# Kernel tuning notes

Measured on AMD Instinct MI355X. Metric: run time of the kernel, lower is better.

## Reference

```python
import jax, jax.numpy as jnp
import numpy as np

H = 256        # hidden_size
MAX_LEN = 200  # position table has MAX_LEN+1 rows
B = 4096       # number of sessions


def setup_inputs() -> dict:
    rng = np.random.RandomState(0)
    # ragged session lengths in [10, 100)
    seq_len = rng.randint(10, 100, size=B).astype(np.int64)
    T = int(seq_len.sum())
    # reverse positions: len-1, ..., 1, 0 per session (as the torch code uses)
    reverse_pos = np.concatenate([np.arange(l - 1, -1, -1) for l in seq_len]).astype(np.int64)

    key = jax.random.key(0)
    ks = jax.random.split(key, 8)
    def lin(k, fin, fout):
        # torch Linear init ~ U(-1/sqrt(fin), 1/sqrt(fin)); store as [fin, fout]
        lim = 1.0 / np.sqrt(fin)
        kw, kb = jax.random.split(k)
        W = jax.random.uniform(kw, (fin, fout), jnp.float32, -lim, lim)
        b = jax.random.uniform(kb, (fout,), jnp.float32, -lim, lim)
        return W, b

    hidden = jax.random.normal(ks[0], (T, H), jnp.float32)
    pos_table = jax.random.normal(ks[1], (MAX_LEN + 1, H), jnp.float32)
    W_pos, b_pos = lin(ks[2], 2 * H, H)   # W_pos_inter
    W1, b1 = lin(ks[3], H, H)             # W_1_inter
    W2, b2 = lin(ks[4], H, H)             # W_2_inter
    qw, qb = lin(ks[5], H, 1)             # q_inter

    return {
        "hidden": hidden,
        "pos_table": pos_table,
        "W_pos": W_pos, "b_pos": b_pos,
        "W1": W1, "b1": b1,
        "W2": W2, "b2": b2,
        "qw": qw, "qb": qb,
        "seq_len": jnp.asarray(seq_len),
        "reverse_pos": jnp.asarray(reverse_pos),
    }


def reference(hidden, pos_table, W_pos, b_pos, W1, b1, W2, b2, qw, qb, seq_len, reverse_pos):
    T = hidden.shape[0]
    nb = seq_len.shape[0]
    # segment id per token (sessions are contiguous)
    seg = jnp.repeat(jnp.arange(nb), seq_len, total_repeat_length=T)  # [T]
    # per-session mean, gathered back per token (v_mean_repeat_concat)
    sess_mean = jax.ops.segment_sum(hidden, seg, num_segments=nb)
    sess_mean = sess_mean / seq_len[:, None].astype(hidden.dtype)
    v_mean = sess_mean[seg]                                           # [T, H]
    # position-augmented hidden: tanh(W_pos_inter([hidden; pos_emb]))
    pos_emb = pos_table[reverse_pos]                                  # [T, H]
    pos_hidden = jnp.tanh(jnp.concatenate([hidden, pos_emb], -1) @ W_pos + b_pos)
    # alpha = q_inter(sigmoid(W_1_inter(v_mean) + W_2_inter(pos_hidden)))
    gate = jax.nn.sigmoid(v_mean @ W1 + b1 + pos_hidden @ W2 + b2)
    alpha = gate @ qw + qb                                            # [T, 1]
    # per-session weighted sum of hidden
    h_s = jax.ops.segment_sum(alpha * hidden, seg, num_segments=nb)   # [B, H]
    return h_s
```

## Files before the change

kernel.cpp:

```cpp
#include <hip/hip_runtime.h>
#include <hip/hip_bf16.h>
#include <stdint.h>

#define HD 256
#define BM 64
#define APAD 8
#define ASTRIDE (HD + APAD)

typedef __bf16 bf16x8 __attribute__((ext_vector_type(8)));
typedef float f32x4 __attribute__((ext_vector_type(4)));
typedef unsigned short ushort8v __attribute__((ext_vector_type(8)));
typedef unsigned short us4 __attribute__((ext_vector_type(4)));

__device__ __forceinline__ unsigned short f2bf(float f) {
    unsigned int x = __float_as_uint(f);
    unsigned int r = (x + 0x7FFFu + ((x >> 16) & 1u)) >> 16;
    return (unsigned short)r;
}

__global__ void prep_kernel(const int* __restrict__ seq_len, int* __restrict__ offsets, int B,
                            const float* __restrict__ Wp, const float* __restrict__ W1,
                            const float* __restrict__ W2,
                            unsigned short* __restrict__ WphT, unsigned short* __restrict__ WpbT,
                            unsigned short* __restrict__ W1T, unsigned short* __restrict__ W2T) {
    int tid = threadIdx.x;
    if (blockIdx.x == 0) {
        __shared__ int sums[256];
        int per = (B + 255) / 256;
        int b0 = tid * per;
        int local[32];
        int tot = 0;
        for (int i = 0; i < per && i < 32; ++i) {
            int b = b0 + i;
            int v = (b < B) ? seq_len[b] : 0;
            local[i] = tot;
            tot += v;
        }
        sums[tid] = tot;
        __syncthreads();
        for (int off = 1; off < 256; off <<= 1) {
            int v = (tid >= off) ? sums[tid - off] : 0;
            __syncthreads();
            sums[tid] += v;
            __syncthreads();
        }
        int start = sums[tid] - tot;
        for (int i = 0; i < per && i < 32; ++i) {
            int b = b0 + i;
            if (b < B) offsets[b] = start + local[i];
        }
        if (tid == 255) offsets[B] = sums[255];
    } else {
        __shared__ unsigned short tile[64][72];
        int bid = blockIdx.x - 1;
        const float* src;
        unsigned short* dst;
        int k0, n0, kk;
        if (bid < 32) {
            int tk = bid >> 2, tn = bid & 3;
            src = Wp; k0 = tk * 64; n0 = tn * 64;
            if (k0 < 256) { dst = WphT; kk = k0; }
            else          { dst = WpbT; kk = k0 - 256; }
        } else if (bid < 48) {
            int b2 = bid - 32;
            src = W1; k0 = (b2 >> 2) * 64; n0 = (b2 & 3) * 64;
            dst = W1T; kk = k0;
        } else {
            int b2 = bid - 48;
            src = W2; k0 = (b2 >> 2) * 64; n0 = (b2 & 3) * 64;
            dst = W2T; kk = k0;
        }
        {
            int col = tid & 63;
            int rbase = tid >> 6;
            #pragma unroll
            for (int i = 0; i < 16; ++i) {
                int lrow = rbase + 4 * i;
                tile[lrow][col] = f2bf(src[(size_t)(k0 + lrow) * HD + n0 + col]);
            }
        }
        __syncthreads();
        {
            int nl = tid >> 2;
            int kc0 = (tid & 3) * 16;
            #pragma unroll
            for (int j = 0; j < 4; ++j) {
                int kc = kc0 + 4 * j;
                us4 v;
                v[0] = tile[kc + 0][nl];
                v[1] = tile[kc + 1][nl];
                v[2] = tile[kc + 2][nl];
                v[3] = tile[kc + 3][nl];
                *reinterpret_cast<us4*>(dst + (size_t)(n0 + nl) * HD + kk + kc) = v;
            }
        }
    }
}

__global__ __launch_bounds__(256) void mean_kernel(
    const float* __restrict__ hidden, const int* __restrict__ offsets,
    unsigned short* __restrict__ mean_bf, unsigned short* __restrict__ hb,
    int* __restrict__ seg, int B) {
    int wave = threadIdx.x >> 6, lane = threadIdx.x & 63;
    int b = blockIdx.x * 4 + wave;
    if (b >= B) return;
    int s = offsets[b], e = offsets[b + 1];
    for (int t = s + lane; t < e; t += 64) seg[t] = b;
    int c4 = lane * 4;
    float4 acc = {0.f, 0.f, 0.f, 0.f};
    if (hb) {
        for (int t = s; t < e; ++t) {
            const float4 v = *reinterpret_cast<const float4*>(hidden + (size_t)t * HD + c4);
            acc.x += v.x; acc.y += v.y; acc.z += v.z; acc.w += v.w;
            us4 pk;
            pk[0] = f2bf(v.x); pk[1] = f2bf(v.y); pk[2] = f2bf(v.z); pk[3] = f2bf(v.w);
            *reinterpret_cast<us4*>(hb + (size_t)t * HD + c4) = pk;
        }
    } else {
        for (int t = s; t < e; ++t) {
            const float4 v = *reinterpret_cast<const float4*>(hidden + (size_t)t * HD + c4);
            acc.x += v.x; acc.y += v.y; acc.z += v.z; acc.w += v.w;
        }
    }
    float inv = 1.0f / (float)(e - s);
    us4 pk;
    pk[0] = f2bf(acc.x * inv);
    pk[1] = f2bf(acc.y * inv);
    pk[2] = f2bf(acc.z * inv);
    pk[3] = f2bf(acc.w * inv);
    *reinterpret_cast<us4*>(mean_bf + (size_t)b * HD + c4) = pk;
}

__global__ __launch_bounds__(256) void small_gemm_kernel(
    const unsigned short* __restrict__ mean_bf, int Mu, int nbu,
    const float* __restrict__ pos_table, int Mp,
    const unsigned short* __restrict__ W1T, const unsigned short* __restrict__ WpbT,
    const float* __restrict__ b1, const float* __restrict__ b2, const float* __restrict__ bp,
    float* __restrict__ u, float* __restrict__ P2) {
    __shared__ __align__(16) unsigned short As[16][ASTRIDE];
    int tid = threadIdx.x;
    bool isU = (int)blockIdx.x < nbu;
    int m0 = isU ? blockIdx.x * 16 : (blockIdx.x - nbu) * 16;
    int M  = isU ? Mu : Mp;
    const unsigned short* BT = isU ? W1T : WpbT;
    float* out = isU ? u : P2;

    {
        int row = tid >> 4;
        int colg = (tid & 15) * 16;
        int m = m0 + row;
        if (isU) {
            ushort8v v0 = {0,0,0,0,0,0,0,0}, v1 = {0,0,0,0,0,0,0,0};
            if (m < M) {
                v0 = *reinterpret_cast<const ushort8v*>(mean_bf + (size_t)m * HD + colg);
                v1 = *reinterpret_cast<const ushort8v*>(mean_bf + (size_t)m * HD + colg + 8);
            }
            *reinterpret_cast<ushort8v*>(&As[row][colg])     = v0;
            *reinterpret_cast<ushort8v*>(&As[row][colg + 8]) = v1;
        } else {
            float4 f[4] = {{0,0,0,0},{0,0,0,0},{0,0,0,0},{0,0,0,0}};
            if (m < M) {
                const float4* p = reinterpret_cast<const float4*>(pos_table + (size_t)m * HD + colg);
                f[0] = p[0]; f[1] = p[1]; f[2] = p[2]; f[3] = p[3];
            }
            ushort8v v0, v1;
            v0[0]=f2bf(f[0].x); v0[1]=f2bf(f[0].y); v0[2]=f2bf(f[0].z); v0[3]=f2bf(f[0].w);
            v0[4]=f2bf(f[1].x); v0[5]=f2bf(f[1].y); v0[6]=f2bf(f[1].z); v0[7]=f2bf(f[1].w);
            v1[0]=f2bf(f[2].x); v1[1]=f2bf(f[2].y); v1[2]=f2bf(f[2].z); v1[3]=f2bf(f[2].w);
            v1[4]=f2bf(f[3].x); v1[5]=f2bf(f[3].y); v1[6]=f2bf(f[3].z); v1[7]=f2bf(f[3].w);
            *reinterpret_cast<ushort8v*>(&As[row][colg])     = v0;
            *reinterpret_cast<ushort8v*>(&As[row][colg + 8]) = v1;
        }
    }
    __syncthreads();

    int wave = tid >> 6, lane = tid & 63, quad = lane >> 4, cc = lane & 15;
    int nb = wave * 64;
    f32x4 acc4[4];
    for (int i = 0; i < 4; ++i) acc4[i] = (f32x4){0.f, 0.f, 0.f, 0.f};

    bf16x8 wfp[4];
    for (int nf = 0; nf < 4; ++nf)
        wfp[nf] = *reinterpret_cast<const bf16x8*>(BT + (size_t)(nb + nf * 16 + cc) * HD + quad * 8);
    for (int kc8 = 0; kc8 < 8; ++kc8) {
        int kc = kc8 * 32;
        bf16x8 wfc[4];
        for (int nf = 0; nf < 4; ++nf) wfc[nf] = wfp[nf];
        if (kc8 < 7)
            for (int nf = 0; nf < 4; ++nf)
                wfp[nf] = *reinterpret_cast<const bf16x8*>(BT + (size_t)(nb + nf * 16 + cc) * HD + kc + 32 + quad * 8);
        bf16x8 af = *reinterpret_cast<const bf16x8*>(&As[cc][kc + quad * 8]);
        for (int nf = 0; nf < 4; ++nf)
            acc4[nf] = __builtin_amdgcn_mfma_f32_16x16x32_bf16(af, wfc[nf], acc4[nf], 0, 0, 0);
    }
    for (int nf = 0; nf < 4; ++nf)
        for (int r = 0; r < 4; ++r) {
            int row = m0 + quad * 4 + r;
            int col = nb + nf * 16 + cc;
            if (row < M) {
                float bias = isU ? (b1[col] + b2[col]) : bp[col];
                out[(size_t)row * HD + col] = acc4[nf][r] + bias;
            }
        }
}

__global__ __launch_bounds__(512, 4) void main_kernel(
    const float* __restrict__ hidden, const unsigned short* __restrict__ hb, int T,
    const unsigned short* __restrict__ WphT,
    const unsigned short* __restrict__ W2T,
    const float* __restrict__ P2,
    const float* __restrict__ u,
    const float* __restrict__ qw, const float* __restrict__ qb,
    const int* __restrict__ rp, const int* __restrict__ seg,
    float* __restrict__ alpha) {
    __shared__ __align__(16) unsigned short Ah[BM][ASTRIDE];
    __shared__ int rp_s[BM];
    __shared__ int seg_s[BM];
    __shared__ float alpha_s[BM];

    int tid = threadIdx.x;
    int t0 = blockIdx.x * BM;
    int wave = tid >> 6, lane = tid & 63, quad = lane >> 4, cc = lane & 15;
    int mb = wave * 32;

    bf16x8 afp[2];
    #pragma unroll
    for (int mf = 0; mf < 2; ++mf)
        afp[mf] = *reinterpret_cast<const bf16x8*>(WphT + (size_t)(mb + mf * 16 + cc) * HD + quad * 8);

    {
        int row = tid >> 3;
        int t = t0 + row;
        if (hb) {
            #pragma unroll
            for (int i = 0; i < 4; ++i) {
                int cg = (tid & 7) * 8 + 64 * i;
                ushort8v v = {0,0,0,0,0,0,0,0};
                if (t < T) v = *reinterpret_cast<const ushort8v*>(hb + (size_t)t * HD + cg);
                *reinterpret_cast<ushort8v*>(&Ah[row][cg]) = v;
            }
        } else {
            #pragma unroll
            for (int i = 0; i < 4; ++i) {
                int cg = (tid & 7) * 8 + 64 * i;
                float4 f0 = {0,0,0,0}, f1 = {0,0,0,0};
                if (t < T) {
                    const float4* p = reinterpret_cast<const float4*>(hidden + (size_t)t * HD + cg);
                    f0 = p[0]; f1 = p[1];
                }
                ushort8v pk;
                pk[0] = f2bf(f0.x); pk[1] = f2bf(f0.y); pk[2] = f2bf(f0.z); pk[3] = f2bf(f0.w);
                pk[4] = f2bf(f1.x); pk[5] = f2bf(f1.y); pk[6] = f2bf(f1.z); pk[7] = f2bf(f1.w);
                *reinterpret_cast<ushort8v*>(&Ah[row][cg]) = pk;
            }
        }
    }
    if (tid < BM) {
        int t = t0 + tid;
        rp_s[tid]  = (t < T) ? rp[t] : 0;
        seg_s[tid] = (t < T) ? seg[t] : 0;
        alpha_s[tid] = qb[0];
    }
    __syncthreads();

    f32x4 acc[2][4];
    #pragma unroll
    for (int i = 0; i < 2; ++i)
        #pragma unroll
        for (int j = 0; j < 4; ++j) acc[i][j] = (f32x4){0.f, 0.f, 0.f, 0.f};

    for (int kc8 = 0; kc8 < 8; ++kc8) {
        int kc = kc8 * 32;
        bf16x8 afc[2];
        #pragma unroll
        for (int mf = 0; mf < 2; ++mf) afc[mf] = afp[mf];
        if (kc8 < 7)
            #pragma unroll
            for (int mf = 0; mf < 2; ++mf)
                afp[mf] = *reinterpret_cast<const bf16x8*>(WphT + (size_t)(mb + mf * 16 + cc) * HD + kc + 32 + quad * 8);
        bf16x8 bfr[4];
        #pragma unroll
        for (int nf = 0; nf < 4; ++nf)
            bfr[nf] = *reinterpret_cast<const bf16x8*>(&Ah[nf * 16 + cc][kc + quad * 8]);
        #pragma unroll
        for (int mf = 0; mf < 2; ++mf)
            #pragma unroll
            for (int nf = 0; nf < 4; ++nf)
                acc[mf][nf] = __builtin_amdgcn_mfma_f32_16x16x32_bf16(afc[mf], bfr[nf], acc[mf][nf], 0, 0, 0);
    }

    f32x4 p2v[4][2];
    #pragma unroll
    for (int nf = 0; nf < 4; ++nf) {
        const float* p2row = P2 + (size_t)rp_s[nf * 16 + cc] * HD;
        #pragma unroll
        for (int mf = 0; mf < 2; ++mf)
            p2v[nf][mf] = *reinterpret_cast<const f32x4*>(p2row + mb + mf * 16 + quad * 4);
    }
    __syncthreads();

    bf16x8 wfp[2];
    #pragma unroll
    for (int mf = 0; mf < 2; ++mf)
        wfp[mf] = *reinterpret_cast<const bf16x8*>(W2T + (size_t)(mb + mf * 16 + cc) * HD + quad * 8);

    #pragma unroll
    for (int nf = 0; nf < 4; ++nf) {
        int token = nf * 16 + cc;
        #pragma unroll
        for (int mf = 0; mf < 2; ++mf) {
            int h0 = mb + mf * 16 + quad * 4;
            us4 pk;
            {
                float v0 = acc[mf][nf][0] + p2v[nf][mf][0];
                float v1 = acc[mf][nf][1] + p2v[nf][mf][1];
                float v2 = acc[mf][nf][2] + p2v[nf][mf][2];
                float v3 = acc[mf][nf][3] + p2v[nf][mf][3];
                float e0 = __expf(2.f * v0), e1 = __expf(2.f * v1);
                float e2 = __expf(2.f * v2), e3 = __expf(2.f * v3);
                pk[0] = f2bf(1.f - 2.f / (e0 + 1.f));
                pk[1] = f2bf(1.f - 2.f / (e1 + 1.f));
                pk[2] = f2bf(1.f - 2.f / (e2 + 1.f));
                pk[3] = f2bf(1.f - 2.f / (e3 + 1.f));
            }
            *reinterpret_cast<us4*>(&Ah[token][h0]) = pk;
            acc[mf][nf] = (f32x4){0.f, 0.f, 0.f, 0.f};
        }
    }
    __syncthreads();

    f32x4 uv[4][2];
    #pragma unroll
    for (int nf = 0; nf < 4; ++nf) {
        const float* urow = u + (size_t)seg_s[nf * 16 + cc] * HD;
        #pragma unroll
        for (int mf = 0; mf < 2; ++mf)
            uv[nf][mf] = *reinterpret_cast<const f32x4*>(urow + mb + mf * 16 + quad * 4);
    }
    f32x4 qv[2];
    #pragma unroll
    for (int mf = 0; mf < 2; ++mf)
        qv[mf] = *reinterpret_cast<const f32x4*>(qw + mb + mf * 16 + quad * 4);

    for (int kc8 = 0; kc8 < 8; ++kc8) {
        int kc = kc8 * 32;
        bf16x8 wfc[2];
        #pragma unroll
        for (int mf = 0; mf < 2; ++mf) wfc[mf] = wfp[mf];
        if (kc8 < 7)
            #pragma unroll
            for (int mf = 0; mf < 2; ++mf)
                wfp[mf] = *reinterpret_cast<const bf16x8*>(W2T + (size_t)(mb + mf * 16 + cc) * HD + kc + 32 + quad * 8);
        #pragma unroll
        for (int nf = 0; nf < 4; ++nf) {
            bf16x8 af = *reinterpret_cast<const bf16x8*>(&Ah[nf * 16 + cc][kc + quad * 8]);
            #pragma unroll
            for (int mf = 0; mf < 2; ++mf)
                acc[mf][nf] = __builtin_amdgcn_mfma_f32_16x16x32_bf16(wfc[mf], af, acc[mf][nf], 0, 0, 0);
        }
    }

    #pragma unroll
    for (int nf = 0; nf < 4; ++nf) {
        int token = nf * 16 + cc;
        float s = 0.f;
        #pragma unroll
        for (int mf = 0; mf < 2; ++mf) {
            #pragma unroll
            for (int r = 0; r < 4; ++r) {
                float g = acc[mf][nf][r] + uv[nf][mf][r];
                g = 1.0f / (1.0f + __expf(-g));
                s += g * qv[mf][r];
            }
        }
        s += __shfl_xor(s, 16);
        s += __shfl_xor(s, 32);
        if (quad == 0) atomicAdd(&alpha_s[token], s);
    }
    __syncthreads();
    if (tid < BM) {
        int t = t0 + tid;
        if (t < T) alpha[t] = alpha_s[tid];
    }
}

__global__ __launch_bounds__(256) void hs_kernel(
    const float* __restrict__ hidden, const unsigned short* __restrict__ hb,
    const float* __restrict__ alpha,
    const int* __restrict__ offsets, float* __restrict__ out, int B) {
    int wave = threadIdx.x >> 6, lane = threadIdx.x & 63;
    int b = blockIdx.x * 4 + wave;
    if (b >= B) return;
    int s = offsets[b], e = offsets[b + 1];
    int c4 = lane * 4;
    float4 acc = {0.f, 0.f, 0.f, 0.f};
    if (hb) {
        for (int t = s; t < e; ++t) {
            float a = alpha[t];
            us4 v = *reinterpret_cast<const us4*>(hb + (size_t)t * HD + c4);
            acc.x += a * __uint_as_float(((unsigned)v[0]) << 16);
            acc.y += a * __uint_as_float(((unsigned)v[1]) << 16);
            acc.z += a * __uint_as_float(((unsigned)v[2]) << 16);
            acc.w += a * __uint_as_float(((unsigned)v[3]) << 16);
        }
    } else {
        for (int t = s; t < e; ++t) {
            float a = alpha[t];
            const float4 v = *reinterpret_cast<const float4*>(hidden + (size_t)t * HD + c4);
            acc.x += a * v.x; acc.y += a * v.y; acc.z += a * v.z; acc.w += a * v.w;
        }
    }
    *reinterpret_cast<float4*>(out + (size_t)b * HD + c4) = acc;
}

extern "C" void kernel_launch(void* const* d_in, const int* in_sizes, int n_in,
                              void* d_out, int out_size, void* d_ws, size_t ws_size,
                              hipStream_t stream) {
    (void)n_in; (void)out_size;
    const float* hidden    = (const float*)d_in[0];
    const float* pos_table = (const float*)d_in[1];
    const float* W_pos     = (const float*)d_in[2];
    const float* b_pos     = (const float*)d_in[3];
    const float* W1        = (const float*)d_in[4];
    const float* b1        = (const float*)d_in[5];
    const float* W2        = (const float*)d_in[6];
    const float* b2        = (const float*)d_in[7];
    const float* qw        = (const float*)d_in[8];
    const float* qb        = (const float*)d_in[9];
    const int* seq_len     = (const int*)d_in[10];
    const int* reverse_pos = (const int*)d_in[11];

    int T  = in_sizes[0] / HD;
    int B  = in_sizes[10];
    int NP = in_sizes[1] / HD;

    char* ws = (char*)d_ws;
    char* ws_end = ws + ws_size;
    auto carve = [&](size_t bytes) -> char* {
        char* p = ws;
        ws += (bytes + 255) & ~(size_t)255;
        return p;
    };
    int* offsets          = (int*)carve((size_t)(B + 1) * sizeof(int));
    int* seg              = (int*)carve((size_t)T * sizeof(int));
    unsigned short* meanb = (unsigned short*)carve((size_t)B * HD * 2);
    float* u              = (float*)carve((size_t)B * HD * sizeof(float));
    float* P2             = (float*)carve((size_t)NP * HD * sizeof(float));
    unsigned short* WphT  = (unsigned short*)carve((size_t)HD * HD * 2);
    unsigned short* WpbT  = (unsigned short*)carve((size_t)HD * HD * 2);
    unsigned short* W1T   = (unsigned short*)carve((size_t)HD * HD * 2);
    unsigned short* W2T   = (unsigned short*)carve((size_t)HD * HD * 2);
    float* alpha          = (float*)carve((size_t)T * sizeof(float));
    unsigned short* hb    = nullptr;
    if ((size_t)(ws_end - ws) >= (size_t)T * HD * 2 + 256)
        hb = (unsigned short*)carve((size_t)T * HD * 2);

    int nbu = (B + 15) / 16;
    int nbp = (NP + 15) / 16;
    int nsb = (B + 3) / 4;

    prep_kernel<<<65, 256, 0, stream>>>(seq_len, offsets, B, W_pos, W1, W2,
                                        WphT, WpbT, W1T, W2T);
    mean_kernel<<<nsb, 256, 0, stream>>>(hidden, offsets, meanb, hb, seg, B);
    small_gemm_kernel<<<nbu + nbp, 256, 0, stream>>>(meanb, B, nbu, pos_table, NP,
                                                     W1T, WpbT, b1, b2, b_pos, u, P2);
    main_kernel<<<(T + BM - 1) / BM, 512, 0, stream>>>(hidden, hb, T, WphT, W2T, P2, u, qw, qb,
                                                       reverse_pos, seg, alpha);
    hs_kernel<<<nsb, 256, 0, stream>>>(hidden, hb, alpha, offsets, (float*)d_out, B);
}
```

Baseline: 578.3 us.

## Fuse mean, u-GEMM and weighted session sum into session-grouped main kernel

Packs whole sessions into 128-row tiles (at most 16 sessions per tile) in the prep kernel, then computes session means, the W1 projection of those means, the gate, alpha and the per-session weighted sum inside one main kernel. This removes the separate mean, small GEMM and hs kernels along with the bf16 hidden copy and the seg/alpha/u intermediates in global memory, cutting launches and HBM round trips. In exchange tiles are partly empty because of packing, the grid launches B blocks and most of them exit early, and the final weighted sum rereads fp32 hidden from global memory.

After: 569.0 us. About the same (-1.6%).

```diff
diff --git a/kernel.cpp b/kernel.cpp
--- a/kernel.cpp
+++ b/kernel.cpp
@@ -3,9 +3,11 @@
 #include <stdint.h>
 
 #define HD 256
-#define BM 64
+#define BM 128
+#define MAXS 16
 #define APAD 8
 #define ASTRIDE (HD + APAD)
+#define USTRIDE (HD + 4)
 
 typedef __bf16 bf16x8 __attribute__((ext_vector_type(8)));
 typedef float f32x4 __attribute__((ext_vector_type(4)));
@@ -17,8 +19,12 @@
     unsigned int r = (x + 0x7FFFu + ((x >> 16) & 1u)) >> 16;
     return (unsigned short)r;
 }
+__device__ __forceinline__ float bf2f(unsigned short u) {
+    return __uint_as_float(((unsigned)u) << 16);
+}
 
 __global__ void prep_kernel(const int* __restrict__ seq_len, int* __restrict__ offsets, int B,
+                            int* __restrict__ grp_off, int* __restrict__ grp_meta,
                             const float* __restrict__ Wp, const float* __restrict__ W1,
                             const float* __restrict__ W2,
                             unsigned short* __restrict__ WphT, unsigned short* __restrict__ WpbT,
@@ -50,6 +56,32 @@
             if (b < B) offsets[b] = start + local[i];
         }
         if (tid == 255) offsets[B] = sums[255];
+
+        int starts[32];
+        int ng = 0;
+        {
+            int cur = 0, cnt = 0;
+            for (int i = 0; i < per && i < 32; ++i) {
+                int b = b0 + i;
+                if (b >= B) break;
+                int nxt = (i + 1 < per && i + 1 < 32) ? local[i + 1] : tot;
+                int len = nxt - local[i];
+                if (i == 0 || cur + len > BM || cnt == MAXS) { starts[ng++] = b; cur = 0; cnt = 0; }
+                cur += len; cnt++;
+            }
+        }
+        __syncthreads();
+        sums[tid] = ng;
+        __syncthreads();
+        for (int off = 1; off < 256; off <<= 1) {
+            int v = (tid >= off) ? sums[tid - off] : 0;
+            __syncthreads();
+            sums[tid] += v;
+            __syncthreads();
+        }
+        int gbase = sums[tid] - ng;
+        for (int j = 0; j < ng; ++j) grp_off[gbase + j] = starts[j];
+        if (tid == 255) { grp_meta[0] = sums[255]; grp_off[sums[255]] = B; }
     } else {
         __shared__ unsigned short tile[64][72];
         int bid = blockIdx.x - 1;
@@ -97,80 +129,29 @@
     }
 }
 
-__global__ __launch_bounds__(256) void mean_kernel(
-    const float* __restrict__ hidden, const int* __restrict__ offsets,
-    unsigned short* __restrict__ mean_bf, unsigned short* __restrict__ hb,
-    int* __restrict__ seg, int B) {
-    int wave = threadIdx.x >> 6, lane = threadIdx.x & 63;
-    int b = blockIdx.x * 4 + wave;
-    if (b >= B) return;
-    int s = offsets[b], e = offsets[b + 1];
-    for (int t = s + lane; t < e; t += 64) seg[t] = b;
-    int c4 = lane * 4;
-    float4 acc = {0.f, 0.f, 0.f, 0.f};
-    if (hb) {
-        for (int t = s; t < e; ++t) {
-            const float4 v = *reinterpret_cast<const float4*>(hidden + (size_t)t * HD + c4);
-            acc.x += v.x; acc.y += v.y; acc.z += v.z; acc.w += v.w;
-            us4 pk;
-            pk[0] = f2bf(v.x); pk[1] = f2bf(v.y); pk[2] = f2bf(v.z); pk[3] = f2bf(v.w);
-            *reinterpret_cast<us4*>(hb + (size_t)t * HD + c4) = pk;
-        }
-    } else {
-        for (int t = s; t < e; ++t) {
-            const float4 v = *reinterpret_cast<const float4*>(hidden + (size_t)t * HD + c4);
-            acc.x += v.x; acc.y += v.y; acc.z += v.z; acc.w += v.w;
-        }
-    }
-    float inv = 1.0f / (float)(e - s);
-    us4 pk;
-    pk[0] = f2bf(acc.x * inv);
-    pk[1] = f2bf(acc.y * inv);
-    pk[2] = f2bf(acc.z * inv);
-    pk[3] = f2bf(acc.w * inv);
-    *reinterpret_cast<us4*>(mean_bf + (size_t)b * HD + c4) = pk;
-}
-
-__global__ __launch_bounds__(256) void small_gemm_kernel(
-    const unsigned short* __restrict__ mean_bf, int Mu, int nbu,
+__global__ __launch_bounds__(256) void p2_kernel(
     const float* __restrict__ pos_table, int Mp,
-    const unsigned short* __restrict__ W1T, const unsigned short* __restrict__ WpbT,
-    const float* __restrict__ b1, const float* __restrict__ b2, const float* __restrict__ bp,
-    float* __restrict__ u, float* __restrict__ P2) {
+    const unsigned short* __restrict__ WpbT, const float* __restrict__ bp,
+    float* __restrict__ P2) {
     __shared__ __align__(16) unsigned short As[16][ASTRIDE];
     int tid = threadIdx.x;
-    bool isU = (int)blockIdx.x < nbu;
-    int m0 = isU ? blockIdx.x * 16 : (blockIdx.x - nbu) * 16;
-    int M  = isU ? Mu : Mp;
-    const unsigned short* BT = isU ? W1T : WpbT;
-    float* out = isU ? u : P2;
-
+    int m0 = blockIdx.x * 16;
     {
         int row = tid >> 4;
         int colg = (tid & 15) * 16;
         int m = m0 + row;
-        if (isU) {
-            ushort8v v0 = {0,0,0,0,0,0,0,0}, v1 = {0,0,0,0,0,0,0,0};
-            if (m < M) {
-                v0 = *reinterpret_cast<const ushort8v*>(mean_bf + (size_t)m * HD + colg);
-                v1 = *reinterpret_cast<const ushort8v*>(mean_bf + (size_t)m * HD + colg + 8);
-            }
-            *reinterpret_cast<ushort8v*>(&As[row][colg])     = v0;
-            *reinterpret_cast<ushort8v*>(&As[row][colg + 8]) = v1;
-        } else {
-            float4 f[4] = {{0,0,0,0},{0,0,0,0},{0,0,0,0},{0,0,0,0}};
-            if (m < M) {
-                const float4* p = reinterpret_cast<const float4*>(pos_table + (size_t)m * HD + colg);
-                f[0] = p[0]; f[1] = p[1]; f[2] = p[2]; f[3] = p[3];
-            }
-            ushort8v v0, v1;
-            v0[0]=f2bf(f[0].x); v0[1]=f2bf(f[0].y); v0[2]=f2bf(f[0].z); v0[3]=f2bf(f[0].w);
-            v0[4]=f2bf(f[1].x); v0[5]=f2bf(f[1].y); v0[6]=f2bf(f[1].z); v0[7]=f2bf(f[1].w);
-            v1[0]=f2bf(f[2].x); v1[1]=f2bf(f[2].y); v1[2]=f2bf(f[2].z); v1[3]=f2bf(f[2].w);
-            v1[4]=f2bf(f[3].x); v1[5]=f2bf(f[3].y); v1[6]=f2bf(f[3].z); v1[7]=f2bf(f[3].w);
-            *reinterpret_cast<ushort8v*>(&As[row][colg])     = v0;
-            *reinterpret_cast<ushort8v*>(&As[row][colg + 8]) = v1;
-        }
+        float4 f[4] = {{0,0,0,0},{0,0,0,0},{0,0,0,0},{0,0,0,0}};
+        if (m < Mp) {
+            const float4* p = reinterpret_cast<const float4*>(pos_table + (size_t)m * HD + colg);
+            f[0] = p[0]; f[1] = p[1]; f[2] = p[2]; f[3] = p[3];
+        }
+        ushort8v v0, v1;
+        v0[0]=f2bf(f[0].x); v0[1]=f2bf(f[0].y); v0[2]=f2bf(f[0].z); v0[3]=f2bf(f[0].w);
+        v0[4]=f2bf(f[1].x); v0[5]=f2bf(f[1].y); v0[6]=f2bf(f[1].z); v0[7]=f2bf(f[1].w);
+        v1[0]=f2bf(f[2].x); v1[1]=f2bf(f[2].y); v1[2]=f2bf(f[2].z); v1[3]=f2bf(f[2].w);
+        v1[4]=f2bf(f[3].x); v1[5]=f2bf(f[3].y); v1[6]=f2bf(f[3].z); v1[7]=f2bf(f[3].w);
+        *reinterpret_cast<ushort8v*>(&As[row][colg])     = v0;
+        *reinterpret_cast<ushort8v*>(&As[row][colg + 8]) = v1;
     }
     __syncthreads();
 
@@ -178,17 +159,16 @@
     int nb = wave * 64;
     f32x4 acc4[4];
     for (int i = 0; i < 4; ++i) acc4[i] = (f32x4){0.f, 0.f, 0.f, 0.f};
-
     bf16x8 wfp[4];
     for (int nf = 0; nf < 4; ++nf)
-        wfp[nf] = *reinterpret_cast<const bf16x8*>(BT + (size_t)(nb + nf * 16 + cc) * HD + quad * 8);
+        wfp[nf] = *reinterpret_cast<const bf16x8*>(WpbT + (size_t)(nb + nf * 16 + cc) * HD + quad * 8);
     for (int kc8 = 0; kc8 < 8; ++kc8) {
         int kc = kc8 * 32;
         bf16x8 wfc[4];
         for (int nf = 0; nf < 4; ++nf) wfc[nf] = wfp[nf];
         if (kc8 < 7)
             for (int nf = 0; nf < 4; ++nf)
-                wfp[nf] = *reinterpret_cast<const bf16x8*>(BT + (size_t)(nb + nf * 16 + cc) * HD + kc + 32 + quad * 8);
+                wfp[nf] = *reinterpret_cast<const bf16x8*>(WpbT + (size_t)(nb + nf * 16 + cc) * HD + kc + 32 + quad * 8);
         bf16x8 af = *reinterpret_cast<const bf16x8*>(&As[cc][kc + quad * 8]);
         for (int nf = 0; nf < 4; ++nf)
             acc4[nf] = __builtin_amdgcn_mfma_f32_16x16x32_bf16(af, wfc[nf], acc4[nf], 0, 0, 0);
@@ -197,31 +177,45 @@
         for (int r = 0; r < 4; ++r) {
             int row = m0 + quad * 4 + r;
             int col = nb + nf * 16 + cc;
-            if (row < M) {
-                float bias = isU ? (b1[col] + b2[col]) : bp[col];
-                out[(size_t)row * HD + col] = acc4[nf][r] + bias;
-            }
+            if (row < Mp) P2[(size_t)row * HD + col] = acc4[nf][r] + bp[col];
         }
 }
 
 __global__ __launch_bounds__(512, 4) void main_kernel(
-    const float* __restrict__ hidden, const unsigned short* __restrict__ hb, int T,
+    const float* __restrict__ hidden,
     const unsigned short* __restrict__ WphT,
+    const unsigned short* __restrict__ W1T,
     const unsigned short* __restrict__ W2T,
     const float* __restrict__ P2,
-    const float* __restrict__ u,
+    const float* __restrict__ b1, const float* __restrict__ b2,
     const float* __restrict__ qw, const float* __restrict__ qb,
-    const int* __restrict__ rp, const int* __restrict__ seg,
-    float* __restrict__ alpha) {
+    const int* __restrict__ rp, const int* __restrict__ offsets,
+    const int* __restrict__ grp_off, const int* __restrict__ grp_meta,
+    float* __restrict__ out) {
     __shared__ __align__(16) unsigned short Ah[BM][ASTRIDE];
+    __shared__ __align__(16) unsigned short Ms[MAXS][ASTRIDE];
+    __shared__ float alpha_s[BM];
     __shared__ int rp_s[BM];
-    __shared__ int seg_s[BM];
-    __shared__ float alpha_s[BM];
-
+    __shared__ int seg_l[BM];
+    __shared__ int sess_st[MAXS + 1];
+
+    int NG = grp_meta[0];
+    if ((int)blockIdx.x >= NG) return;
     int tid = threadIdx.x;
-    int t0 = blockIdx.x * BM;
-    int wave = tid >> 6, lane = tid & 63, quad = lane >> 4, cc = lane & 15;
-    int mb = wave * 32;
+    int b0  = grp_off[blockIdx.x];
+    int b1e = grp_off[blockIdx.x + 1];
+    int nsess = b1e - b0;
+    int t0g = offsets[b0];
+    int nrows = offsets[b1e] - t0g;
+
+    int wv = tid >> 6, lane = tid & 63, quad = lane >> 4, cc = lane & 15;
+    int mb = wv * 32;
+
+    if (tid <= nsess) sess_st[tid] = offsets[b0 + tid] - t0g;
+    if (tid < BM) {
+        alpha_s[tid] = qb[0];
+        rp_s[tid] = (tid < nrows) ? rp[t0g + tid] : 0;
+    }
 
     bf16x8 afp[2];
     #pragma unroll
@@ -229,93 +223,99 @@
         afp[mf] = *reinterpret_cast<const bf16x8*>(WphT + (size_t)(mb + mf * 16 + cc) * HD + quad * 8);
 
     {
-        int row = tid >> 3;
-        int t = t0 + row;
-        if (hb) {
-            #pragma unroll
-            for (int i = 0; i < 4; ++i) {
-                int cg = (tid & 7) * 8 + 64 * i;
-                ushort8v v = {0,0,0,0,0,0,0,0};
-                if (t < T) v = *reinterpret_cast<const ushort8v*>(hb + (size_t)t * HD + cg);
-                *reinterpret_cast<ushort8v*>(&Ah[row][cg]) = v;
-            }
-        } else {
-            #pragma unroll
-            for (int i = 0; i < 4; ++i) {
-                int cg = (tid & 7) * 8 + 64 * i;
-                float4 f0 = {0,0,0,0}, f1 = {0,0,0,0};
-                if (t < T) {
-                    const float4* p = reinterpret_cast<const float4*>(hidden + (size_t)t * HD + cg);
-                    f0 = p[0]; f1 = p[1];
-                }
-                ushort8v pk;
-                pk[0] = f2bf(f0.x); pk[1] = f2bf(f0.y); pk[2] = f2bf(f0.z); pk[3] = f2bf(f0.w);
-                pk[4] = f2bf(f1.x); pk[5] = f2bf(f1.y); pk[6] = f2bf(f1.z); pk[7] = f2bf(f1.w);
-                *reinterpret_cast<ushort8v*>(&Ah[row][cg]) = pk;
-            }
-        }
-    }
+        int row = tid >> 2;
+        #pragma unroll
+        for (int i = 0; i < 8; ++i) {
+            int cg = (tid & 3) * 8 + 32 * i;
+            float4 f0 = {0,0,0,0}, f1 = {0,0,0,0};
+            if (row < nrows) {
+                const float4* p = reinterpret_cast<const float4*>(hidden + (size_t)(t0g + row) * HD + cg);
+                f0 = p[0]; f1 = p[1];
+            }
+            ushort8v pk;
+            pk[0] = f2bf(f0.x); pk[1] = f2bf(f0.y); pk[2] = f2bf(f0.z); pk[3] = f2bf(f0.w);
+            pk[4] = f2bf(f1.x); pk[5] = f2bf(f1.y); pk[6] = f2bf(f1.z); pk[7] = f2bf(f1.w);
+            *reinterpret_cast<ushort8v*>(&Ah[row][cg]) = pk;
+        }
+    }
+    __syncthreads();
+
     if (tid < BM) {
-        int t = t0 + tid;
-        rp_s[tid]  = (t < T) ? rp[t] : 0;
-        seg_s[tid] = (t < T) ? seg[t] : 0;
-        alpha_s[tid] = qb[0];
-    }
-    __syncthreads();
-
-    f32x4 acc[2][4];
+        int s = 0;
+        #pragma unroll
+        for (int stp = 8; stp >= 1; stp >>= 1)
+            if (s + stp < nsess && sess_st[s + stp] <= tid) s += stp;
+        seg_l[tid] = (tid < nrows) ? s : 0;
+    }
+    for (int s = wv; s < nsess; s += 8) {
+        int st = sess_st[s], en = sess_st[s + 1];
+        float a0 = 0.f, a1 = 0.f, a2 = 0.f, a3 = 0.f;
+        for (int r = st; r < en; ++r) {
+            us4 v = *reinterpret_cast<const us4*>(&Ah[r][lane * 4]);
+            a0 += bf2f(v[0]); a1 += bf2f(v[1]); a2 += bf2f(v[2]); a3 += bf2f(v[3]);
+        }
+        float inv = 1.0f / (float)(en - st);
+        us4 pk;
+        pk[0] = f2bf(a0 * inv); pk[1] = f2bf(a1 * inv);
+        pk[2] = f2bf(a2 * inv); pk[3] = f2bf(a3 * inv);
+        *reinterpret_cast<us4*>(&Ms[s][lane * 4]) = pk;
+    }
+    __syncthreads();
+
+    f32x4 acc[2][8];
     #pragma unroll
     for (int i = 0; i < 2; ++i)
         #pragma unroll
-        for (int j = 0; j < 4; ++j) acc[i][j] = (f32x4){0.f, 0.f, 0.f, 0.f};
+        for (int j = 0; j < 8; ++j) acc[i][j] = (f32x4){0.f, 0.f, 0.f, 0.f};
 
     for (int kc8 = 0; kc8 < 8; ++kc8) {
         int kc = kc8 * 32;
-        bf16x8 afc[2];
-        #pragma unroll
-        for (int mf = 0; mf < 2; ++mf) afc[mf] = afp[mf];
+        bf16x8 afc[2] = {afp[0], afp[1]};
         if (kc8 < 7)
             #pragma unroll
             for (int mf = 0; mf < 2; ++mf)
                 afp[mf] = *reinterpret_cast<const bf16x8*>(WphT + (size_t)(mb + mf * 16 + cc) * HD + kc + 32 + quad * 8);
-        bf16x8 bfr[4];
-        #pragma unroll
-        for (int nf = 0; nf < 4; ++nf)
-            bfr[nf] = *reinterpret_cast<const bf16x8*>(&Ah[nf * 16 + cc][kc + quad * 8]);
-        #pragma unroll
-        for (int mf = 0; mf < 2; ++mf)
-            #pragma unroll
-            for (int nf = 0; nf < 4; ++nf)
-                acc[mf][nf] = __builtin_amdgcn_mfma_f32_16x16x32_bf16(afc[mf], bfr[nf], acc[mf][nf], 0, 0, 0);
-    }
-
-    f32x4 p2v[4][2];
-    #pragma unroll
-    for (int nf = 0; nf < 4; ++nf) {
-        const float* p2row = P2 + (size_t)rp_s[nf * 16 + cc] * HD;
-        #pragma unroll
-        for (int mf = 0; mf < 2; ++mf)
-            p2v[nf][mf] = *reinterpret_cast<const f32x4*>(p2row + mb + mf * 16 + quad * 4);
-    }
-    __syncthreads();
+        #pragma unroll
+        for (int nf = 0; nf < 8; ++nf) {
+            bf16x8 bfr = *reinterpret_cast<const bf16x8*>(&Ah[nf * 16 + cc][kc + quad * 8]);
+            acc[0][nf] = __builtin_amdgcn_mfma_f32_16x16x32_bf16(afc[0], bfr, acc[0][nf], 0, 0, 0);
+            acc[1][nf] = __builtin_amdgcn_mfma_f32_16x16x32_bf16(afc[1], bfr, acc[1][nf], 0, 0, 0);
+        }
+    }
+
+    f32x4 uacc[2];
+    uacc[0] = (f32x4){0.f, 0.f, 0.f, 0.f};
+    uacc[1] = (f32x4){0.f, 0.f, 0.f, 0.f};
+    for (int kc8 = 0; kc8 < 8; ++kc8) {
+        int kc = kc8 * 32;
+        bf16x8 msf = *reinterpret_cast<const bf16x8*>(&Ms[cc][kc + quad * 8]);
+        #pragma unroll
+        for (int nf = 0; nf < 2; ++nf) {
+            bf16x8 wf = *reinterpret_cast<const bf16x8*>(W1T + (size_t)(mb + nf * 16 + cc) * HD + kc + quad * 8);
+            uacc[nf] = __builtin_amdgcn_mfma_f32_16x16x32_bf16(msf, wf, uacc[nf], 0, 0, 0);
+        }
+    }
 
     bf16x8 wfp[2];
     #pragma unroll
     for (int mf = 0; mf < 2; ++mf)
         wfp[mf] = *reinterpret_cast<const bf16x8*>(W2T + (size_t)(mb + mf * 16 + cc) * HD + quad * 8);
-
-    #pragma unroll
-    for (int nf = 0; nf < 4; ++nf) {
+    __syncthreads();
+
+    #pragma unroll
+    for (int nf = 0; nf < 8; ++nf) {
         int token = nf * 16 + cc;
+        const float* p2row = P2 + (size_t)rp_s[token] * HD;
         #pragma unroll
         for (int mf = 0; mf < 2; ++mf) {
             int h0 = mb + mf * 16 + quad * 4;
+            const f32x4 p2v = *reinterpret_cast<const f32x4*>(p2row + h0);
             us4 pk;
             {
-                float v0 = acc[mf][nf][0] + p2v[nf][mf][0];
-                float v1 = acc[mf][nf][1] + p2v[nf][mf][1];
-                float v2 = acc[mf][nf][2] + p2v[nf][mf][2];
-                float v3 = acc[mf][nf][3] + p2v[nf][mf][3];
+                float v0 = acc[mf][nf][0] + p2v[0];
+                float v1 = acc[mf][nf][1] + p2v[1];
+                float v2 = acc[mf][nf][2] + p2v[2];
+                float v3 = acc[mf][nf][3] + p2v[3];
                 float e0 = __expf(2.f * v0), e1 = __expf(2.f * v1);
                 float e2 = __expf(2.f * v2), e3 = __expf(2.f * v3);
                 pk[0] = f2bf(1.f - 2.f / (e0 + 1.f));
@@ -329,46 +329,50 @@
     }
     __syncthreads();
 
-    f32x4 uv[4][2];
-    #pragma unroll
-    for (int nf = 0; nf < 4; ++nf) {
-        const float* urow = u + (size_t)seg_s[nf * 16 + cc] * HD;
-        #pragma unroll
-        for (int mf = 0; mf < 2; ++mf)
-            uv[nf][mf] = *reinterpret_cast<const f32x4*>(urow + mb + mf * 16 + quad * 4);
-    }
+    for (int kc8 = 0; kc8 < 8; ++kc8) {
+        int kc = kc8 * 32;
+        bf16x8 wfc[2] = {wfp[0], wfp[1]};
+        if (kc8 < 7)
+            #pragma unroll
+            for (int mf = 0; mf < 2; ++mf)
+                wfp[mf] = *reinterpret_cast<const bf16x8*>(W2T + (size_t)(mb + mf * 16 + cc) * HD + kc + 32 + quad * 8);
+        #pragma unroll
+        for (int nf = 0; nf < 8; ++nf) {
+            bf16x8 af = *reinterpret_cast<const bf16x8*>(&Ah[nf * 16 + cc][kc + quad * 8]);
+            acc[0][nf] = __builtin_amdgcn_mfma_f32_16x16x32_bf16(wfc[0], af, acc[0][nf], 0, 0, 0);
+            acc[1][nf] = __builtin_amdgcn_mfma_f32_16x16x32_bf16(wfc[1], af, acc[1][nf], 0, 0, 0);
+        }
+    }
+    __syncthreads();
+
+    float* usp = reinterpret_cast<float*>(&Ah[0][0]);
+    {
+        #pragma unroll
+        for (int nf = 0; nf < 2; ++nf) {
+            int n = mb + nf * 16 + cc;
+            float b12 = b1[n] + b2[n];
+            #pragma unroll
+            for (int r = 0; r < 4; ++r)
+                usp[(quad * 4 + r) * USTRIDE + n] = uacc[nf][r] + b12;
+        }
+    }
+    __syncthreads();
+
     f32x4 qv[2];
     #pragma unroll
     for (int mf = 0; mf < 2; ++mf)
         qv[mf] = *reinterpret_cast<const f32x4*>(qw + mb + mf * 16 + quad * 4);
-
-    for (int kc8 = 0; kc8 < 8; ++kc8) {
-        int kc = kc8 * 32;
-        bf16x8 wfc[2];
-        #pragma unroll
-        for (int mf = 0; mf < 2; ++mf) wfc[mf] = wfp[mf];
-        if (kc8 < 7)
-            #pragma unroll
-            for (int mf = 0; mf < 2; ++mf)
-                wfp[mf] = *reinterpret_cast<const bf16x8*>(W2T + (size_t)(mb + mf * 16 + cc) * HD + kc + 32 + quad * 8);
-        #pragma unroll
-        for (int nf = 0; nf < 4; ++nf) {
-            bf16x8 af = *reinterpret_cast<const bf16x8*>(&Ah[nf * 16 + cc][kc + quad * 8]);
-            #pragma unroll
-            for (int mf = 0; mf < 2; ++mf)
-                acc[mf][nf] = __builtin_amdgcn_mfma_f32_16x16x32_bf16(wfc[mf], af, acc[mf][nf], 0, 0, 0);
-        }
-    }
-
-    #pragma unroll
-    for (int nf = 0; nf < 4; ++nf) {
+    #pragma unroll
+    for (int nf = 0; nf < 8; ++nf) {
         int token = nf * 16 + cc;
+        int stok = seg_l[token];
         float s = 0.f;
         #pragma unroll
         for (int mf = 0; mf < 2; ++mf) {
+            const f32x4 uv = *reinterpret_cast<const f32x4*>(&usp[stok * USTRIDE + mb + mf * 16 + quad * 4]);
             #pragma unroll
             for (int r = 0; r < 4; ++r) {
-                float g = acc[mf][nf][r] + uv[nf][mf][r];
+                float g = acc[mf][nf][r] + uv[r];
                 g = 1.0f / (1.0f + __expf(-g));
                 s += g * qv[mf][r];
             }
@@ -378,45 +382,28 @@
         if (quad == 0) atomicAdd(&alpha_s[token], s);
     }
     __syncthreads();
-    if (tid < BM) {
-        int t = t0 + tid;
-        if (t < T) alpha[t] = alpha_s[tid];
-    }
-}
-
-__global__ __launch_bounds__(256) void hs_kernel(
-    const float* __restrict__ hidden, const unsigned short* __restrict__ hb,
-    const float* __restrict__ alpha,
-    const int* __restrict__ offsets, float* __restrict__ out, int B) {
-    int wave = threadIdx.x >> 6, lane = threadIdx.x & 63;
-    int b = blockIdx.x * 4 + wave;
-    if (b >= B) return;
-    int s = offsets[b], e = offsets[b + 1];
-    int c4 = lane * 4;
-    float4 acc = {0.f, 0.f, 0.f, 0.f};
-    if (hb) {
-        for (int t = s; t < e; ++t) {
-            float a = alpha[t];
-            us4 v = *reinterpret_cast<const us4*>(hb + (size_t)t * HD + c4);
-            acc.x += a * __uint_as_float(((unsigned)v[0]) << 16);
-            acc.y += a * __uint_as_float(((unsigned)v[1]) << 16);
-            acc.z += a * __uint_as_float(((unsigned)v[2]) << 16);
-            acc.w += a * __uint_as_float(((unsigned)v[3]) << 16);
-        }
-    } else {
-        for (int t = s; t < e; ++t) {
-            float a = alpha[t];
-            const float4 v = *reinterpret_cast<const float4*>(hidden + (size_t)t * HD + c4);
-            acc.x += a * v.x; acc.y += a * v.y; acc.z += a * v.z; acc.w += a * v.w;
-        }
-    }
-    *reinterpret_cast<float4*>(out + (size_t)b * HD + c4) = acc;
+
+    {
+        int col = tid & 255, p = tid >> 8;
+        const float* hp = hidden + (size_t)t0g * HD + col;
+        for (int si = p; si < nsess; si += 2) {
+            int st = sess_st[si], en = sess_st[si + 1];
+            float a0 = 0.f, a1 = 0.f;
+            int r = st;
+            for (; r + 1 < en; r += 2) {
+                a0 += alpha_s[r]     * hp[(size_t)r * HD];
+                a1 += alpha_s[r + 1] * hp[(size_t)(r + 1) * HD];
+            }
+            if (r < en) a0 += alpha_s[r] * hp[(size_t)r * HD];
+            out[(size_t)(b0 + si) * HD + col] = a0 + a1;
+        }
+    }
 }
 
 extern "C" void kernel_launch(void* const* d_in, const int* in_sizes, int n_in,
                               void* d_out, int out_size, void* d_ws, size_t ws_size,
                               hipStream_t stream) {
-    (void)n_in; (void)out_size;
+    (void)n_in; (void)out_size; (void)ws_size;
     const float* hidden    = (const float*)d_in[0];
     const float* pos_table = (const float*)d_in[1];
     const float* W_pos     = (const float*)d_in[2];
@@ -430,41 +417,28 @@
     const int* seq_len     = (const int*)d_in[10];
     const int* reverse_pos = (const int*)d_in[11];
 
-    int T  = in_sizes[0] / HD;
     int B  = in_sizes[10];
     int NP = in_sizes[1] / HD;
 
     char* ws = (char*)d_ws;
-    char* ws_end = ws + ws_size;
     auto carve = [&](size_t bytes) -> char* {
         char* p = ws;
         ws += (bytes + 255) & ~(size_t)255;
         return p;
     };
     int* offsets          = (int*)carve((size_t)(B + 1) * sizeof(int));
-    int* seg              = (int*)carve((size_t)T * sizeof(int));
-    unsigned short* meanb = (unsigned short*)carve((size_t)B * HD * 2);
-    float* u              = (float*)carve((size_t)B * HD * sizeof(float));
+    int* grp_off          = (int*)carve((size_t)(B + 2) * sizeof(int));
+    int* grp_meta         = (int*)carve(64);
     float* P2             = (float*)carve((size_t)NP * HD * sizeof(float));
     unsigned short* WphT  = (unsigned short*)carve((size_t)HD * HD * 2);
     unsigned short* WpbT  = (unsigned short*)carve((size_t)HD * HD * 2);
     unsigned short* W1T   = (unsigned short*)carve((size_t)HD * HD * 2);
     unsigned short* W2T   = (unsigned short*)carve((size_t)HD * HD * 2);
-    float* alpha          = (float*)carve((size_t)T * sizeof(float));
-    unsigned short* hb    = nullptr;
-    if ((size_t)(ws_end - ws) >= (size_t)T * HD * 2 + 256)
-        hb = (unsigned short*)carve((size_t)T * HD * 2);
-
-    int nbu = (B + 15) / 16;
-    int nbp = (NP + 15) / 16;
-    int nsb = (B + 3) / 4;
-
-    prep_kernel<<<65, 256, 0, stream>>>(seq_len, offsets, B, W_pos, W1, W2,
-                                        WphT, WpbT, W1T, W2T);
-    mean_kernel<<<nsb, 256, 0, stream>>>(hidden, offsets, meanb, hb, seg, B);
-    small_gemm_kernel<<<nbu + nbp, 256, 0, stream>>>(meanb, B, nbu, pos_table, NP,
-                                                     W1T, WpbT, b1, b2, b_pos, u, P2);
-    main_kernel<<<(T + BM - 1) / BM, 512, 0, stream>>>(hidden, hb, T, WphT, W2T, P2, u, qw, qb,
-                                                       reverse_pos, seg, alpha);
-    hs_kernel<<<nsb, 256, 0, stream>>>(hidden, hb, alpha, offsets, (float*)d_out, B);
-}
+
+    prep_kernel<<<65, 256, 0, stream>>>(seq_len, offsets, B, grp_off, grp_meta,
+                                        W_pos, W1, W2, WphT, WpbT, W1T, W2T);
+    p2_kernel<<<(NP + 15) / 16, 256, 0, stream>>>(pos_table, NP, WpbT, b_pos, P2);
+    main_kernel<<<B, 512, 0, stream>>>(hidden, WphT, W1T, W2T, P2, b1, b2, qw, qb,
+                                       reverse_pos, offsets, grp_off, grp_meta,
+                                       (float*)d_out);
+}
```
